# Performance work log

Hardware: AMD Instinct MI355X
Metric: run time of the kernel (lower is better)

The kernel has to match this reference:

```python
import jax, jax.numpy as jnp
import numpy as np

N_HEAD = 12
LN_EPS = 1e-5


def setup_inputs() -> dict:
    key = jax.random.key(0)
    ks = jax.random.split(key, 4)
    B, T, C = 4, 2048, 768
    s = C ** -0.5
    return {
        "x": jax.random.normal(ks[0], (B, T, C), jnp.float32),
        "w_attn": jax.random.normal(ks[1], (C, 3 * C), jnp.float32) * s,
        "b_attn": jnp.zeros((3 * C,), jnp.float32),
        "w_proj": jax.random.normal(ks[2], (C, C), jnp.float32) * s,
        "b_proj": jnp.zeros((C,), jnp.float32),
        "ln1_g": jnp.ones((C,), jnp.float32),
        "ln1_b": jnp.zeros((C,), jnp.float32),
        "ln2_g": jnp.ones((C,), jnp.float32),
        "ln2_b": jnp.zeros((C,), jnp.float32),
    }


def _layernorm(x, g, b):
    mu = jnp.mean(x, axis=-1, keepdims=True)
    var = jnp.mean(jnp.square(x - mu), axis=-1, keepdims=True)
    return (x - mu) * jax.lax.rsqrt(var + LN_EPS) * g + b


def _attn(h, w_attn, b_attn, w_proj, b_proj):
    B, T, C = h.shape
    hd = C // N_HEAD
    # Faithful to torch: view(B,T,H,3*hd) then split 3*hd -> q,k,v per head
    qkv = (h @ w_attn + b_attn).reshape(B, T, N_HEAD, 3, hd)
    q = jnp.transpose(qkv[:, :, :, 0, :], (0, 2, 1, 3))  # (B,H,T,hd)
    k = jnp.transpose(qkv[:, :, :, 1, :], (0, 2, 1, 3))
    v = jnp.transpose(qkv[:, :, :, 2, :], (0, 2, 1, 3))
    # NOTE: scale is C**-0.5 (full embed dim) and there is NO causal mask,
    # exactly as in the source.
    scores = jnp.einsum("bhtd,bhsd->bhts", q, k) * (C ** -0.5)
    a = jax.nn.softmax(scores, axis=-1)
    y = jnp.einsum("bhts,bhsd->bhtd", a, v)
    y = jnp.transpose(y, (0, 2, 1, 3)).reshape(B, T, C)
    return y @ w_proj + b_proj


def reference(x, w_attn, b_attn, w_proj, b_proj, ln1_g, ln1_b, ln2_g, ln2_b):
    # Faithful to source Block.forward: attn applied twice, MLP never called.
    x = x + _attn(_layernorm(x, ln1_g, ln1_b), w_attn, b_attn, w_proj, b_proj)
    x = x + _attn(_layernorm(x, ln2_g, ln2_b), w_attn, b_attn, w_proj, b_proj)
    return x
```

## Files before the change

### kernel.cpp

```cpp
#include <hip/hip_runtime.h>


using bf16x8 = __attribute__((ext_vector_type(8))) short;
using f32x4  = __attribute__((ext_vector_type(4))) float;

__device__ __forceinline__ unsigned short f2b(float f) {
  unsigned u = __builtin_bit_cast(unsigned, f);
  u += 0x7FFFu + ((u >> 16) & 1u);
  return (unsigned short)(u >> 16);
}
__device__ __forceinline__ unsigned pk2(float a, float b) {
  unsigned ua = __builtin_bit_cast(unsigned, a);
  ua += 0x7FFFu + ((ua >> 16) & 1u);
  unsigned ub = __builtin_bit_cast(unsigned, b);
  ub += 0x7FFFu + ((ub >> 16) & 1u);
  return (ua >> 16) | (ub & 0xFFFF0000u);
}

#define ASYNC16(g, l)                                                        \
  __builtin_amdgcn_global_load_lds(                                          \
      (const __attribute__((address_space(1))) void*)(g),                    \
      (__attribute__((address_space(3))) void*)(l), 16, 0, 0)

__global__ __launch_bounds__(256) void wt_kernel(const float* __restrict__ w,
                                                 unsigned short* __restrict__ wt,
                                                 int N) {
  __shared__ float tile[32][33];
  const int n0 = blockIdx.x * 32, k0 = blockIdx.y * 32;
  const int tx = threadIdx.x, ty = threadIdx.y;
#pragma unroll
  for (int i = 0; i < 32; i += 8)
    tile[ty + i][tx] = w[(size_t)(k0 + ty + i) * N + n0 + tx];
  __syncthreads();
#pragma unroll
  for (int i = 0; i < 32; i += 8)
    wt[(size_t)(n0 + ty + i) * 768 + k0 + tx] = f2b(tile[tx][ty + i]);
}

__global__ __launch_bounds__(256) void ln_kernel(const float* __restrict__ x,
                                                 const float* __restrict__ g,
                                                 const float* __restrict__ b,
                                                 unsigned short* __restrict__ h) {
  __shared__ float red[8];
  const int row = blockIdx.x;
  const int tid = threadIdx.x;
  const float* xr = x + (size_t)row * 768;
  float v0 = xr[tid], v1 = xr[tid + 256], v2 = xr[tid + 512];
  float s = v0 + v1 + v2;
  float s2 = v0 * v0 + v1 * v1 + v2 * v2;
#pragma unroll
  for (int off = 1; off < 64; off <<= 1) {
    s += __shfl_xor(s, off);
    s2 += __shfl_xor(s2, off);
  }
  if ((tid & 63) == 0) { red[tid >> 6] = s; red[4 + (tid >> 6)] = s2; }
  __syncthreads();
  const float S  = red[0] + red[1] + red[2] + red[3];
  const float S2 = red[4] + red[5] + red[6] + red[7];
  const float mu  = S * (1.0f / 768.0f);
  const float var = S2 * (1.0f / 768.0f) - mu * mu;
  const float inv = rsqrtf(var + 1e-5f);
  unsigned short* hr = h + (size_t)row * 768;
  hr[tid]       = f2b((v0 - mu) * inv * g[tid] + b[tid]);
  hr[tid + 256] = f2b((v1 - mu) * inv * g[tid + 256] + b[tid + 256]);
  hr[tid + 512] = f2b((v2 - mu) * inv * g[tid + 512] + b[tid + 512]);
}

template <int EPI>
__global__ __launch_bounds__(256, 2) void gemm_kernel(
    const unsigned short* __restrict__ A, const unsigned short* __restrict__ Bt,
    const float* __restrict__ bias, const float* __restrict__ resid,
    unsigned short* __restrict__ q, unsigned short* __restrict__ k,
    unsigned short* __restrict__ v, float* __restrict__ outF) {
  __shared__ alignas(16) unsigned short As[128 * 32];
  __shared__ alignas(16) unsigned short Bs[128 * 32];

  const int tid = threadIdx.x;
  const int wv = tid >> 6;
  const int lane = tid & 63;
  const int quad = lane >> 4;
  const int l15 = lane & 15;
  const int m0 = blockIdx.y * 128;
  const int n0 = blockIdx.x * 128;

  const int o0 = wv * 1024 + lane * 16;
  const int rT0 = o0 >> 6, c0 = (o0 & 63) >> 1;
  const int o1 = o0 + 4096;
  const int rT1 = o1 >> 6, c1 = (o1 & 63) >> 1;

  const unsigned short* gA0 = A + (size_t)(m0 + rT0) * 768 + c0;
  const unsigned short* gA1 = A + (size_t)(m0 + rT1) * 768 + c1;
  const unsigned short* gB0 = Bt + (size_t)(n0 + rT0) * 768 + c0;
  const unsigned short* gB1 = Bt + (size_t)(n0 + rT1) * 768 + c1;
  unsigned short* lA0 = &As[wv * 512];
  unsigned short* lA1 = &As[wv * 512 + 2048];
  unsigned short* lB0 = &Bs[wv * 512];
  unsigned short* lB1 = &Bs[wv * 512 + 2048];

  f32x4 acc[4][4];
#pragma unroll
  for (int i = 0; i < 4; ++i)
#pragma unroll
    for (int j = 0; j < 4; ++j) acc[i][j] = {0.f, 0.f, 0.f, 0.f};

  const int mBase = (wv >> 1) * 64;
  const int nBase = (wv & 1) * 64;

  for (int kk = 0; kk < 24; ++kk) {
    const int ko = kk * 32;
    ASYNC16(gA0 + ko, lA0);
    ASYNC16(gA1 + ko, lA1);
    ASYNC16(gB0 + ko, lB0);
    ASYNC16(gB1 + ko, lB1);
    __syncthreads();
    bf16x8 af[4], bfv[4];
#pragma unroll
    for (int mt = 0; mt < 4; ++mt)
      af[mt] = *(const bf16x8*)&As[(mBase + mt * 16 + l15) * 32 + quad * 8];
#pragma unroll
    for (int nt = 0; nt < 4; ++nt)
      bfv[nt] = *(const bf16x8*)&Bs[(nBase + nt * 16 + l15) * 32 + quad * 8];
#pragma unroll
    for (int mt = 0; mt < 4; ++mt)
#pragma unroll
      for (int nt = 0; nt < 4; ++nt)
        acc[mt][nt] = __builtin_amdgcn_mfma_f32_16x16x32_bf16(af[mt], bfv[nt],
                                                              acc[mt][nt], 0, 0, 0);
    __syncthreads();
  }

  if constexpr (EPI == 0) {
#pragma unroll
    for (int mt = 0; mt < 4; ++mt) {
#pragma unroll
      for (int nt = 0; nt < 4; ++nt) {
        const int n = n0 + nBase + nt * 16 + l15;
        const int head = n / 192;
        const int rem = n - head * 192;
        const int sel = rem >> 6;
        const int d = rem & 63;
        unsigned short* tgt = (sel == 0) ? q : (sel == 1) ? k : v;
        const float bv = bias[n];
#pragma unroll
        for (int r = 0; r < 4; ++r) {
          const int m = m0 + mBase + mt * 16 + quad * 4 + r;
          const int bb = m >> 11;
          const int t = m & 2047;
          tgt[(((size_t)bb * 12 + head) * 2048 + t) * 64 + d] =
              f2b(acc[mt][nt][r] + bv);
        }
      }
    }
  } else {
#pragma unroll
    for (int mt = 0; mt < 4; ++mt) {
#pragma unroll
      for (int nt = 0; nt < 4; ++nt) {
        const int n = n0 + nBase + nt * 16 + l15;
        const float bv = bias[n];
#pragma unroll
        for (int r = 0; r < 4; ++r) {
          const int m = m0 + mBase + mt * 16 + quad * 4 + r;
          const size_t idx = (size_t)m * 768 + n;
          outF[idx] = resid[idx] + bv + acc[mt][nt][r];
        }
      }
    }
  }
}

__global__ __launch_bounds__(256) void vtrans_kernel(const unsigned short* __restrict__ V,
                                                     unsigned short* __restrict__ Vt) {
  const int bh = blockIdx.x;
  const int t = blockIdx.y * 256 + threadIdx.x;
  const uint4* s4 = (const uint4*)(V + ((size_t)bh * 2048 + t) * 64);
  const size_t ob = (size_t)bh * 64 * 2048 + t;
#pragma unroll
  for (int i = 0; i < 8; ++i) {
    const uint4 u = s4[i];
    const unsigned w[4] = {u.x, u.y, u.z, u.w};
#pragma unroll
    for (int j = 0; j < 4; ++j) {
      Vt[ob + (size_t)(i * 8 + j * 2) * 2048]     = (unsigned short)(w[j] & 0xFFFFu);
      Vt[ob + (size_t)(i * 8 + j * 2 + 1) * 2048] = (unsigned short)(w[j] >> 16);
    }
  }
}

#define PAD 68
__global__ __launch_bounds__(256, 3) void attn_kernel(
    const unsigned short* __restrict__ Q, const unsigned short* __restrict__ Km,
    const unsigned short* __restrict__ Vt, unsigned short* __restrict__ Y) {
  __shared__ alignas(16) unsigned short Ks[2][64 * PAD];
  __shared__ alignas(16) unsigned short Vs[2][64 * PAD];
  __shared__ alignas(16) unsigned short Ps[4][32 * PAD];

  const int bh = blockIdx.x;
  const int qt = blockIdx.y;
  const int tid = threadIdx.x;
  const int wv = tid >> 6;
  const int lane = tid & 63;
  const int quad = lane >> 4;
  const int l15 = lane & 15;
  const size_t bhT = (size_t)bh * 2048;

  bf16x8 qf[2][2];
#pragma unroll
  for (int g = 0; g < 2; ++g) {
    const unsigned short* qb = Q + (bhT + qt * 128 + wv * 32 + g * 16 + l15) * 64;
    qf[g][0] = *(const bf16x8*)(qb + quad * 8);
    qf[g][1] = *(const bf16x8*)(qb + 32 + quad * 8);
  }

  f32x4 o[4][2], ol[2];
#pragma unroll
  for (int dt = 0; dt < 4; ++dt)
#pragma unroll
    for (int g = 0; g < 2; ++g) o[dt][g] = {0.f, 0.f, 0.f, 0.f};
  ol[0] = {0.f, 0.f, 0.f, 0.f};
  ol[1] = {0.f, 0.f, 0.f, 0.f};
  const bf16x8 ones = {0x3F80, 0x3F80, 0x3F80, 0x3F80,
                       0x3F80, 0x3F80, 0x3F80, 0x3F80};

  const int kr = tid >> 3;
  const int kc = (tid & 7) * 8;
  const unsigned short* gK = Km + (bhT + kr) * 64 + kc;
  const unsigned short* gV = Vt + ((size_t)bh * 64 + kr) * 2048 + kc;
  const int lo0 = kr * PAD + kc;
  const int lo1 = (kr + 32) * PAD + kc;
  const float c2 = 0.052062786090587f;

  bf16x8 sk0 = *(const bf16x8*)(gK);
  bf16x8 sk1 = *(const bf16x8*)(gK + 32 * 64);
  bf16x8 sv0 = *(const bf16x8*)(gV);
  bf16x8 sv1 = *(const bf16x8*)(gV + 32 * 2048);

  for (int c = 0; c < 32; ++c) {
    const int p = c & 1;
    *(bf16x8*)&Ks[p][lo0] = sk0;
    *(bf16x8*)&Ks[p][lo1] = sk1;
    *(bf16x8*)&Vs[p][lo0] = sv0;
    *(bf16x8*)&Vs[p][lo1] = sv1;
    __syncthreads();
    if (c < 31) {
      sk0 = *(const bf16x8*)(gK + (size_t)(c + 1) * 4096);
      sk1 = *(const bf16x8*)(gK + (size_t)(c + 1) * 4096 + 2048);
      sv0 = *(const bf16x8*)(gV + (c + 1) * 64);
      sv1 = *(const bf16x8*)(gV + (c + 1) * 64 + 32 * 2048);
    }

    f32x4 s[2][4];
#pragma unroll
    for (int tt = 0; tt < 4; ++tt) {
      bf16x8 kf0 = *(const bf16x8*)&Ks[p][(tt * 16 + l15) * PAD + quad * 8];
      bf16x8 kf1 = *(const bf16x8*)&Ks[p][(tt * 16 + l15) * PAD + 32 + quad * 8];
      s[0][tt] = {0.f, 0.f, 0.f, 0.f};
      s[1][tt] = {0.f, 0.f, 0.f, 0.f};
      s[0][tt] = __builtin_amdgcn_mfma_f32_16x16x32_bf16(kf0, qf[0][0], s[0][tt], 0, 0, 0);
      s[1][tt] = __builtin_amdgcn_mfma_f32_16x16x32_bf16(kf0, qf[1][0], s[1][tt], 0, 0, 0);
      s[0][tt] = __builtin_amdgcn_mfma_f32_16x16x32_bf16(kf1, qf[0][1], s[0][tt], 0, 0, 0);
      s[1][tt] = __builtin_amdgcn_mfma_f32_16x16x32_bf16(kf1, qf[1][1], s[1][tt], 0, 0, 0);
    }

#pragma unroll
    for (int g = 0; g < 2; ++g)
#pragma unroll
      for (int tt = 0; tt < 4; ++tt) {
        const float e0 = __builtin_amdgcn_exp2f(s[g][tt][0] * c2);
        const float e1 = __builtin_amdgcn_exp2f(s[g][tt][1] * c2);
        const float e2 = __builtin_amdgcn_exp2f(s[g][tt][2] * c2);
        const float e3 = __builtin_amdgcn_exp2f(s[g][tt][3] * c2);
        const unsigned long long pk =
            (unsigned long long)pk2(e0, e1) |
            ((unsigned long long)pk2(e2, e3) << 32);
        *(unsigned long long*)&Ps[wv][(g * 16 + l15) * PAD + tt * 16 + quad * 4] = pk;
      }

#pragma unroll
    for (int ks = 0; ks < 2; ++ks) {
      bf16x8 pf0 = *(const bf16x8*)&Ps[wv][(l15) * PAD + ks * 32 + quad * 8];
      bf16x8 pf1 = *(const bf16x8*)&Ps[wv][(16 + l15) * PAD + ks * 32 + quad * 8];
      ol[0] = __builtin_amdgcn_mfma_f32_16x16x32_bf16(ones, pf0, ol[0], 0, 0, 0);
      ol[1] = __builtin_amdgcn_mfma_f32_16x16x32_bf16(ones, pf1, ol[1], 0, 0, 0);
#pragma unroll
      for (int dt = 0; dt < 4; ++dt) {
        bf16x8 vf = *(const bf16x8*)&Vs[p][(dt * 16 + l15) * PAD + ks * 32 + quad * 8];
        o[dt][0] = __builtin_amdgcn_mfma_f32_16x16x32_bf16(vf, pf0, o[dt][0], 0, 0, 0);
        o[dt][1] = __builtin_amdgcn_mfma_f32_16x16x32_bf16(vf, pf1, o[dt][1], 0, 0, 0);
      }
    }
  }

  const int b = bh / 12;
  const int head = bh - b * 12;
#pragma unroll
  for (int g = 0; g < 2; ++g) {
    const float rl = 1.0f / ol[g][0];
    const int row = qt * 128 + wv * 32 + g * 16 + l15;
    unsigned short* yb = Y + ((size_t)(b * 2048 + row)) * 768 + head * 64;
#pragma unroll
    for (int dt = 0; dt < 4; ++dt) {
      const unsigned long long pk =
          (unsigned long long)pk2(o[dt][g][0] * rl, o[dt][g][1] * rl) |
          ((unsigned long long)pk2(o[dt][g][2] * rl, o[dt][g][3] * rl) << 32);
      *(unsigned long long*)(yb + dt * 16 + quad * 4) = pk;
    }
  }
}

extern "C" void kernel_launch(void* const* d_in, const int* in_sizes, int n_in,
                              void* d_out, int out_size, void* d_ws, size_t ws_size,
                              hipStream_t stream) {
  const float* x      = (const float*)d_in[0];
  const float* w_attn = (const float*)d_in[1];
  const float* b_attn = (const float*)d_in[2];
  const float* w_proj = (const float*)d_in[3];
  const float* b_proj = (const float*)d_in[4];
  const float* ln_g[2] = {(const float*)d_in[5], (const float*)d_in[7]};
  const float* ln_b[2] = {(const float*)d_in[6], (const float*)d_in[8]};
  float* out = (float*)d_out;

  unsigned short* wAt = (unsigned short*)d_ws;
  unsigned short* wPt = wAt + 2304 * 768;
  unsigned short* h   = wPt + 768 * 768;
  unsigned short* q   = h + 8192 * 768;
  unsigned short* k   = q + 48 * 2048 * 64;
  unsigned short* v   = k + 48 * 2048 * 64;
  unsigned short* vt  = v + 48 * 2048 * 64;
  unsigned short* y   = vt + 48 * 2048 * 64;

  wt_kernel<<<dim3(72, 24), dim3(32, 8), 0, stream>>>(w_attn, wAt, 2304);
  wt_kernel<<<dim3(24, 24), dim3(32, 8), 0, stream>>>(w_proj, wPt, 768);

  for (int pass = 0; pass < 2; ++pass) {
    const float* xin = pass ? (const float*)out : x;
    ln_kernel<<<8192, 256, 0, stream>>>(xin, ln_g[pass], ln_b[pass], h);
    gemm_kernel<0><<<dim3(18, 64), 256, 0, stream>>>(h, wAt, b_attn, nullptr,
                                                     q, k, v, nullptr);
    vtrans_kernel<<<dim3(48, 8), 256, 0, stream>>>(v, vt);
    attn_kernel<<<dim3(48, 16), 256, 0, stream>>>(q, k, vt, y);
    gemm_kernel<1><<<dim3(6, 64), 256, 0, stream>>>(y, wPt, b_proj, xin,
                                                    nullptr, nullptr, nullptr, out);
  }
}
```

Before: 410.3 us.

## Fuse V transpose into QKV GEMM epilogue and prescale Q for softmax

The QKV GEMM epilogue now writes V straight into the transposed (d-major) layout with packed 4-element stores, so the separate vtrans kernel and its extra V buffer round trip are removed. The softmax scale constant is folded into Q at GEMM time, which drops one multiply per score in the attention inner loop. The bf16 packing of exp values also switches from round-to-nearest to truncation. These changes trade slightly different rounding in Q and P for less memory traffic and fewer ALU ops.

```diff
diff --git a/kernel.cpp b/kernel.cpp
--- a/kernel.cpp
+++ b/kernel.cpp
@@ -15,6 +15,10 @@
   unsigned ub = __builtin_bit_cast(unsigned, b);
   ub += 0x7FFFu + ((ub >> 16) & 1u);
   return (ua >> 16) | (ub & 0xFFFF0000u);
+}
+__device__ __forceinline__ unsigned pk2t(float a, float b) {
+  return (__builtin_bit_cast(unsigned, a) >> 16) |
+         (__builtin_bit_cast(unsigned, b) & 0xFFFF0000u);
 }
 
 #define ASYNC16(g, l)                                                        \
@@ -71,7 +75,7 @@
     const unsigned short* __restrict__ A, const unsigned short* __restrict__ Bt,
     const float* __restrict__ bias, const float* __restrict__ resid,
     unsigned short* __restrict__ q, unsigned short* __restrict__ k,
-    unsigned short* __restrict__ v, float* __restrict__ outF) {
+    unsigned short* __restrict__ vt, float* __restrict__ outF) {
   __shared__ alignas(16) unsigned short As[128 * 32];
   __shared__ alignas(16) unsigned short Bs[128 * 32];
 
@@ -130,6 +134,7 @@
   }
 
   if constexpr (EPI == 0) {
+    const float c2 = 0.052062786090587f;
 #pragma unroll
     for (int mt = 0; mt < 4; ++mt) {
 #pragma unroll
@@ -139,15 +144,22 @@
         const int rem = n - head * 192;
         const int sel = rem >> 6;
         const int d = rem & 63;
-        unsigned short* tgt = (sel == 0) ? q : (sel == 1) ? k : v;
         const float bv = bias[n];
-#pragma unroll
-        for (int r = 0; r < 4; ++r) {
-          const int m = m0 + mBase + mt * 16 + quad * 4 + r;
-          const int bb = m >> 11;
-          const int t = m & 2047;
-          tgt[(((size_t)bb * 12 + head) * 2048 + t) * 64 + d] =
-              f2b(acc[mt][nt][r] + bv);
+        const int mr = m0 + mBase + mt * 16 + quad * 4;
+        const int bb = mr >> 11;
+        const int t = mr & 2047;
+        if (sel == 2) {
+          const unsigned long long pk =
+              (unsigned long long)pk2(acc[mt][nt][0] + bv, acc[mt][nt][1] + bv) |
+              ((unsigned long long)pk2(acc[mt][nt][2] + bv, acc[mt][nt][3] + bv) << 32);
+          *(unsigned long long*)&vt[(((size_t)bb * 12 + head) * 64 + d) * 2048 + t] = pk;
+        } else {
+          unsigned short* tgt = (sel == 0) ? q : k;
+          const float sc = (sel == 0) ? c2 : 1.0f;
+#pragma unroll
+          for (int r = 0; r < 4; ++r)
+            tgt[(((size_t)bb * 12 + head) * 2048 + t + r) * 64 + d] =
+                f2b((acc[mt][nt][r] + bv) * sc);
         }
       }
     }
@@ -165,24 +177,6 @@
           outF[idx] = resid[idx] + bv + acc[mt][nt][r];
         }
       }
-    }
-  }
-}
-
-__global__ __launch_bounds__(256) void vtrans_kernel(const unsigned short* __restrict__ V,
-                                                     unsigned short* __restrict__ Vt) {
-  const int bh = blockIdx.x;
-  const int t = blockIdx.y * 256 + threadIdx.x;
-  const uint4* s4 = (const uint4*)(V + ((size_t)bh * 2048 + t) * 64);
-  const size_t ob = (size_t)bh * 64 * 2048 + t;
-#pragma unroll
-  for (int i = 0; i < 8; ++i) {
-    const uint4 u = s4[i];
-    const unsigned w[4] = {u.x, u.y, u.z, u.w};
-#pragma unroll
-    for (int j = 0; j < 4; ++j) {
-      Vt[ob + (size_t)(i * 8 + j * 2) * 2048]     = (unsigned short)(w[j] & 0xFFFFu);
-      Vt[ob + (size_t)(i * 8 + j * 2 + 1) * 2048] = (unsigned short)(w[j] >> 16);
     }
   }
 }
@@ -228,7 +222,6 @@
   const unsigned short* gV = Vt + ((size_t)bh * 64 + kr) * 2048 + kc;
   const int lo0 = kr * PAD + kc;
   const int lo1 = (kr + 32) * PAD + kc;
-  const float c2 = 0.052062786090587f;
 
   bf16x8 sk0 = *(const bf16x8*)(gK);
   bf16x8 sk1 = *(const bf16x8*)(gK + 32 * 64);
@@ -266,13 +259,13 @@
     for (int g = 0; g < 2; ++g)
 #pragma unroll
       for (int tt = 0; tt < 4; ++tt) {
-        const float e0 = __builtin_amdgcn_exp2f(s[g][tt][0] * c2);
-        const float e1 = __builtin_amdgcn_exp2f(s[g][tt][1] * c2);
-        const float e2 = __builtin_amdgcn_exp2f(s[g][tt][2] * c2);
-        const float e3 = __builtin_amdgcn_exp2f(s[g][tt][3] * c2);
+        const float e0 = __builtin_amdgcn_exp2f(s[g][tt][0]);
+        const float e1 = __builtin_amdgcn_exp2f(s[g][tt][1]);
+        const float e2 = __builtin_amdgcn_exp2f(s[g][tt][2]);
+        const float e3 = __builtin_amdgcn_exp2f(s[g][tt][3]);
         const unsigned long long pk =
-            (unsigned long long)pk2(e0, e1) |
-            ((unsigned long long)pk2(e2, e3) << 32);
+            (unsigned long long)pk2t(e0, e1) |
+            ((unsigned long long)pk2t(e2, e3) << 32);
         *(unsigned long long*)&Ps[wv][(g * 16 + l15) * PAD + tt * 16 + quad * 4] = pk;
       }
 
@@ -325,8 +318,7 @@
   unsigned short* h   = wPt + 768 * 768;
   unsigned short* q   = h + 8192 * 768;
   unsigned short* k   = q + 48 * 2048 * 64;
-  unsigned short* v   = k + 48 * 2048 * 64;
-  unsigned short* vt  = v + 48 * 2048 * 64;
+  unsigned short* vt  = k + 48 * 2048 * 64;
   unsigned short* y   = vt + 48 * 2048 * 64;
 
   wt_kernel<<<dim3(72, 24), dim3(32, 8), 0, stream>>>(w_attn, wAt, 2304);
@@ -336,8 +328,7 @@
     const float* xin = pass ? (const float*)out : x;
     ln_kernel<<<8192, 256, 0, stream>>>(xin, ln_g[pass], ln_b[pass], h);
     gemm_kernel<0><<<dim3(18, 64), 256, 0, stream>>>(h, wAt, b_attn, nullptr,
-                                                     q, k, v, nullptr);
-    vtrans_kernel<<<dim3(48, 8), 256, 0, stream>>>(v, vt);
+                                                     q, k, vt, nullptr);
     attn_kernel<<<dim3(48, 16), 256, 0, stream>>>(q, k, vt, y);
     gemm_kernel<1><<<dim3(6, 64), 256, 0, stream>>>(y, wPt, b_proj, xin,
                                                     nullptr, nullptr, nullptr, out);
```

Result: faster. 386.5 us (-5.8%).
